# Kernel tuning notes

Measured on AMD Instinct MI355X. Metric: run time of the kernel, lower is better.

The kernel has to match this reference:

```python
import jax, jax.numpy as jnp
import numpy as np
import math

P = 7          # patch / kernel size (must be odd for onion-peeling: N = 1+4*m*(m+1) = P*P)
EPS = 1e-6
EPS_W = 0.5

def _ball_dirs():
    u = [np.array([[1.0, 0.0]])]
    s = [np.zeros(1)]
    for k in range(1, P // 2 + 1):
        n = 8 * k
        th = np.linspace(0.0, 2.0 * math.pi * (1.0 - 1.0 / n), n)
        u.append(np.stack([np.cos(th), np.sin(th)], 1))
        s.append(np.full(n, k / (P // 2)))
    return (np.concatenate(u, 0).astype(np.float32), np.concatenate(s).astype(np.float32))

_U, _S = _ball_dirs()  # [N,2], [N], N == P*P == 49

def _forward(x, metric_w, metric_b, proj_w, proj_b):
    B, C, H, W = x.shape
    Hp, Wp = H // P, W // P
    u = jnp.asarray(_U)
    s = jnp.asarray(_S)
    # metric net: strided conv -> 7 params per patch
    params = jax.lax.conv_general_dilated(
        x, metric_w, (P, P), 'VALID',
        dimension_numbers=('NCHW', 'OIHW', 'NCHW')) + metric_b[None, :, None, None]
    v_raw = jnp.moveaxis(params[:, :2], 1, -1)                      # [B,Hp,Wp,2]
    v = v_raw / jnp.maximum(jnp.linalg.norm(v_raw, axis=-1, keepdims=True), 1e-12)
    eig = 2.0 * jax.nn.sigmoid(jnp.moveaxis(params[:, 2:4], 1, -1))  # [B,Hp,Wp,2]
    scale = 0.5 + 1.5 * jax.nn.sigmoid(jnp.moveaxis(params[:, 4:5], 1, -1))
    eig = eig * scale
    vp = jnp.stack([-v[..., 1], v[..., 0]], -1)
    R = jnp.stack([v, vp], -1)                                      # [B,Hp,Wp,2,2] (columns v, v_perp)
    M = R @ (eig[..., None] * jnp.swapaxes(R, -1, -2))              # R diag(eig) R^T
    w = params[:, 5:7]                                              # [B,2,Hp,Wp]
    w = w * (1.0 - EPS_W) * jax.nn.sigmoid(jnp.linalg.norm(w, axis=1, keepdims=True))
    # Finsler-Randers norm F(u) = sqrt(u^T M u + eps) + w.u for all N unit dirs
    quad = jnp.einsum('nj,bhwij,ni->bnhw', u, M, u)                 # [B,N,Hp,Wp]
    drift = jnp.einsum('bihw,ni->bnhw', w, u)
    F_u = jnp.sqrt(quad + EPS) + drift
    y = (u[None, :, :, None, None] / (F_u[:, :, None] + EPS)
         * s[None, :, None, None, None])                            # [B,N,2,Hp,Wp]
    y = y.reshape(B, P, P, 2, Hp, Wp)[:, :, :, ::-1]                # flip last coord pair (x,y)->(y,x)
    gi = jnp.arange(P, dtype=x.dtype) - P // 2
    grid = jnp.stack(jnp.meshgrid(gi, gi, indexing='ij'), -1)       # [P,P,2]
    off = y - grid[None, :, :, :, None, None]                       # [B,P,P,2,Hp,Wp]
    off_y = jnp.transpose(off[:, :, :, 0], (0, 3, 4, 1, 2))         # [B,Hp,Wp,P,P]
    off_x = jnp.transpose(off[:, :, :, 1], (0, 3, 4, 1, 2))
    base_h = (jnp.arange(Hp, dtype=x.dtype) * P)[None, :, None, None, None]
    base_w = (jnp.arange(Wp, dtype=x.dtype) * P)[None, None, :, None, None]
    ki = jnp.arange(P, dtype=x.dtype)
    py = off_y + base_h + ki[None, None, None, :, None]             # sample rows
    px = off_x + base_w + ki[None, None, None, None, :]             # sample cols
    # bilinear sampling with zero padding (torchvision deform_conv2d semantics)
    y0 = jnp.floor(py)
    x0 = jnp.floor(px)
    wy = py - y0
    wx = px - x0

    def gather(yi, xi):
        valid = (yi >= 0) & (yi <= H - 1) & (xi >= 0) & (xi <= W - 1)
        yc = jnp.clip(yi, 0, H - 1).astype(jnp.int32)
        xc = jnp.clip(xi, 0, W - 1).astype(jnp.int32)
        vals = jax.vmap(lambda img, yy, xx: img[:, yy, xx])(x, yc, xc)  # [B,C,Hp,Wp,P,P]
        return vals * valid[:, None].astype(x.dtype)

    sampled = (gather(y0, x0) * ((1 - wy) * (1 - wx))[:, None]
               + gather(y0, x0 + 1) * ((1 - wy) * wx)[:, None]
               + gather(y0 + 1, x0) * (wy * (1 - wx))[:, None]
               + gather(y0 + 1, x0 + 1) * (wy * wx)[:, None])       # [B,C,Hp,Wp,P,P]
    out = jnp.einsum('bchwij,ecij->behw', sampled, proj_w) + proj_b[None, :, None, None]
    return jnp.moveaxis(out.reshape(B, out.shape[1], -1), 1, 2)     # [B, Hp*Wp, E]

def setup_inputs():
    key = jax.random.key(0)
    k0, k1, k2 = jax.random.split(key, 3)
    B, C, H, W, E = 64, 3, 224, 224, 384
    x = jax.random.normal(k0, (B, C, H, W), jnp.float32)
    metric_w = jax.random.normal(k1, (7, C, P, P), jnp.float32) / math.sqrt(C * P * P)
    metric_b = jnp.zeros((7,), jnp.float32)
    proj_w = jax.random.normal(k2, (E, C, P, P), jnp.float32) / (P * math.sqrt(C))
    proj_b = jnp.zeros((E,), jnp.float32)
    return {"x": x, "metric_w": metric_w, "metric_b": metric_b,
            "proj_w": proj_w, "proj_b": proj_b}

def reference(x, metric_w, metric_b, proj_w, proj_b):
    return _forward(x, metric_w, metric_b, proj_w, proj_b)
```

## Files before the change

### kernel.cpp

```cpp
#include <hip/hip_runtime.h>
#include <math.h>

#define PP   7
#define NDIR 49
#define CIN  3
#define KK   147
#define KPAD 160
#define EE   384
#define HH   224
#define WW   224
#define GG   16
#define TB   256
#define NPX  112
#define WSTR 208
#define SROW 164
#define SSTR 17

typedef __attribute__((ext_vector_type(8))) __bf16 bf16x8;
typedef __attribute__((ext_vector_type(4))) float  f32x4;

__device__ __forceinline__ float sigmoidf_(float v) {
    return 1.0f / (1.0f + expf(-v));
}

__global__ void pack_kernel(const float* __restrict__ x,
                            const float* __restrict__ pw,
                            const float* __restrict__ mw,
                            float* __restrict__ xp,
                            unsigned short* __restrict__ pwB,
                            float* __restrict__ mwg,
                            int npix4) {
    int idx = blockIdx.x * blockDim.x + threadIdx.x;
    if (idx < EE * KPAD) {
        int e = idx / KPAD;
        int k = idx - e * KPAD;
        float v = (k < KK) ? pw[e * KK + k] : 0.0f;
        __bf16 h = (__bf16)v;
        pwB[idx] = *(unsigned short*)&h;
    }
    if (idx < 7 * WSTR) {
        int prm = idx / WSTR, r = idx - prm * WSTR;
        float v = 0.0f;
        if (r < 196) {
            int q = r >> 2, c = r & 3;
            if (c < 3) v = mw[prm * KK + c * 49 + q];
        }
        mwg[idx] = v;
    }
    if (idx < npix4) {
        const int ppi = HH * WW / 4;
        int b = idx / ppi;
        int p = (idx - b * ppi) * 4;
        const float* xb = x + (size_t)b * (CIN * HH * WW) + p;
        f32x4 r0 = *(const f32x4*)(xb);
        f32x4 r1 = *(const f32x4*)(xb + HH * WW);
        f32x4 r2 = *(const f32x4*)(xb + 2 * HH * WW);
        float* op = xp + ((size_t)b * (HH * WW) + p) * 4;
        #pragma unroll
        for (int i = 0; i < 4; ++i) {
            f32x4 v = {r0[i], r1[i], r2[i], 0.0f};
            *(f32x4*)(op + i * 4) = v;
        }
    }
}

__launch_bounds__(TB, 8)
__global__ void fused_kernel(const float* __restrict__ xp,
                             const float* __restrict__ mwg,
                             const float* __restrict__ mb,
                             const unsigned short* __restrict__ pwB,
                             const float* __restrict__ pb,
                             float* __restrict__ out) {
    __shared__ __align__(16) float mwp_s[7 * WSTR];
    __shared__ float dirs[NDIR][3];
    __shared__ float par_s[GG][8];
    __shared__ float der_s[GG][5];
    __shared__ __align__(16) float buf[3136];

    const int t   = threadIdx.x;
    const int blk = blockIdx.x;
    const int b   = blk >> 6;
    const int rem = blk & 63;
    const int hp  = rem >> 1;
    const int wp0 = (rem & 1) * GG;
    const size_t m0 = (size_t)blk * GG;
    const int row0 = hp * PP;
    const int col0 = wp0 * PP;

    for (int i4 = t; i4 < 7 * WSTR / 4; i4 += TB)
        *(f32x4*)&mwp_s[i4 * 4] = *(const f32x4*)&mwg[i4 * 4];
    if (t >= 64 && t < 64 + NDIR) {
        int n = t - 64;
        float u0, u1, s;
        if (n == 0)      { u0 = 1.0f; u1 = 0.0f; s = 0.0f; }
        else if (n < 9)  { float th = (float)(n - 1)  * 0.78539816339744831f; u0 = cosf(th); u1 = sinf(th); s = 0.33333334f; }
        else if (n < 25) { float th = (float)(n - 9)  * 0.39269908169872414f; u0 = cosf(th); u1 = sinf(th); s = 0.66666669f; }
        else             { float th = (float)(n - 25) * 0.26179938779914941f; u0 = cosf(th); u1 = sinf(th); s = 1.0f; }
        dirs[n][0] = u0; dirs[n][1] = u1; dirs[n][2] = s;
    }

    const size_t pbase = (size_t)b * (HH * WW);
    for (int item = t; item < 7 * NPX; item += TB) {
        int i = item / NPX, px = item - i * NPX;
        f32x4 v = *(const f32x4*)(xp + (pbase + (size_t)(row0 + i) * WW + col0 + px) * 4);
        *(f32x4*)&buf[item * 4] = v;
    }
    __syncthreads();

    if (t < 112) {
        int prm = t >> 4, g = t & 15;
        const float* wrow = &mwp_s[prm * WSTR];
        float acc0 = 0.0f, acc1 = 0.0f, acc2 = 0.0f;
        #pragma unroll 1
        for (int i = 0; i < 7; ++i) {
            const float* bp = &buf[(i * NPX + g * 7) * 4];
            const float* wp = &wrow[i * 28];
            #pragma unroll
            for (int j = 0; j < 7; ++j) {
                f32x4 pix = *(const f32x4*)&bp[j * 4];
                f32x4 w4  = *(const f32x4*)&wp[j * 4];
                acc0 = fmaf(pix[0], w4[0], acc0);
                acc1 = fmaf(pix[1], w4[1], acc1);
                acc2 = fmaf(pix[2], w4[2], acc2);
            }
        }
        par_s[g][prm] = mb[prm] + acc0 + acc1 + acc2;
    }
    __syncthreads();

    if (t < GG) {
        float a0 = par_s[t][0], a1 = par_s[t][1], a2 = par_s[t][2], a3 = par_s[t][3];
        float a4 = par_s[t][4], a5 = par_s[t][5], a6 = par_s[t][6];
        float nrm = sqrtf(a0 * a0 + a1 * a1);
        float inv = 1.0f / fmaxf(nrm, 1e-12f);
        float v0 = a0 * inv, v1 = a1 * inv;
        float e0 = 2.0f * sigmoidf_(a2);
        float e1 = 2.0f * sigmoidf_(a3);
        float sc = 0.5f + 1.5f * sigmoidf_(a4);
        e0 *= sc; e1 *= sc;
        float wn  = sqrtf(a5 * a5 + a6 * a6);
        float wsc = 0.5f * sigmoidf_(wn);
        der_s[t][0] = e0 * v0 * v0 + e1 * v1 * v1;
        der_s[t][1] = (e0 - e1) * v0 * v1;
        der_s[t][2] = e0 * v1 * v1 + e1 * v0 * v0;
        der_s[t][3] = a5 * wsc;
        der_s[t][4] = a6 * wsc;
    }
    for (int z = t; z < GG * (SROW - KK); z += TB) {
        int g = z / (SROW - KK), r = z - g * (SROW - KK);
        buf[g * SROW + KK + r] = 0.0f;
    }
    __syncthreads();

    for (int item = t; item < GG * NDIR; item += TB) {
        int g = item / NDIR;
        int n = item - g * NDIR;
        float u0 = dirs[n][0], u1 = dirs[n][1], s = dirs[n][2];
        float M00 = der_s[g][0], M01 = der_s[g][1], M11 = der_s[g][2];
        float w0 = der_s[g][3], w1 = der_s[g][4];
        float quad  = u0 * u0 * M00 + 2.0f * u0 * u1 * M01 + u1 * u1 * M11;
        float drift = w0 * u0 + w1 * u1;
        float F = sqrtf(quad + 1e-6f) + drift;
        float r = s / (F + 1e-6f);
        float py = (float)(row0 + 3) + u1 * r;
        float px = (float)(col0 + g * PP + 3) + u0 * r;
        float y0f = floorf(py), x0f = floorf(px);
        float y1f = y0f + 1.0f, x1f = x0f + 1.0f;
        float wy = py - y0f, wx = px - x0f;
        float c00 = (1.0f - wy) * (1.0f - wx);
        float c01 = (1.0f - wy) * wx;
        float c10 = wy * (1.0f - wx);
        float c11 = wy * wx;
        bool vy0 = (y0f >= 0.0f) && (y0f <= (float)(HH - 1));
        bool vy1 = (y1f >= 0.0f) && (y1f <= (float)(HH - 1));
        bool vx0 = (x0f >= 0.0f) && (x0f <= (float)(WW - 1));
        bool vx1 = (x1f >= 0.0f) && (x1f <= (float)(WW - 1));
        c00 *= (vy0 && vx0) ? 1.0f : 0.0f;
        c01 *= (vy0 && vx1) ? 1.0f : 0.0f;
        c10 *= (vy1 && vx0) ? 1.0f : 0.0f;
        c11 *= (vy1 && vx1) ? 1.0f : 0.0f;
        int iy0 = (int)fminf(fmaxf(y0f, 0.0f), (float)(HH - 1));
        int iy1 = (int)fminf(fmaxf(y1f, 0.0f), (float)(HH - 1));
        int ix0 = (int)fminf(fmaxf(x0f, 0.0f), (float)(WW - 1));
        int ix1 = (int)fminf(fmaxf(x1f, 0.0f), (float)(WW - 1));
        f32x4 q00 = *(const f32x4*)(xp + (pbase + (size_t)(iy0 * WW + ix0)) * 4);
        f32x4 q01 = *(const f32x4*)(xp + (pbase + (size_t)(iy0 * WW + ix1)) * 4);
        f32x4 q10 = *(const f32x4*)(xp + (pbase + (size_t)(iy1 * WW + ix0)) * 4);
        f32x4 q11 = *(const f32x4*)(xp + (pbase + (size_t)(iy1 * WW + ix1)) * 4);
        #pragma unroll
        for (int c = 0; c < CIN; ++c) {
            buf[g * SROW + c * NDIR + n] =
                q00[c] * c00 + q01[c] * c01 + q10[c] * c10 + q11[c] * c11;
        }
    }
    __syncthreads();

    const int lane = t & 63;
    const int wv   = t >> 6;
    const int nrow = lane & 15;
    const int hi   = lane >> 4;

    bf16x8 sfr[5];
    const float* srow = &buf[nrow * SROW];
    #pragma unroll
    for (int ks = 0; ks < 5; ++ks) {
        f32x4 lo = *(const f32x4*)&srow[ks * 32 + hi * 8];
        f32x4 hv = *(const f32x4*)&srow[ks * 32 + hi * 8 + 4];
        #pragma unroll
        for (int j = 0; j < 4; ++j) sfr[ks][j] = (__bf16)lo[j];
        #pragma unroll
        for (int j = 0; j < 4; ++j) sfr[ks][4 + j] = (__bf16)hv[j];
    }

    float* orow = out + (m0 + nrow) * EE;
    #pragma unroll
    for (int q = 0; q < 6; ++q) {
        int tile = wv * 6 + q;
        int erow = tile * 16 + nrow;
        const unsigned short* arow = pwB + (size_t)erow * KPAD + hi * 8;
        f32x4 acc = {0.0f, 0.0f, 0.0f, 0.0f};
        #pragma unroll
        for (int ks = 0; ks < 5; ++ks) {
            bf16x8 afr = *(const bf16x8*)&arow[ks * 32];
            acc = __builtin_amdgcn_mfma_f32_16x16x32_bf16(afr, sfr[ks], acc, 0, 0, 0);
        }
        int e0 = tile * 16 + hi * 4;
        f32x4 b4 = *(const f32x4*)&pb[e0];
        f32x4 o = acc + b4;
        *(f32x4*)&orow[e0] = o;
    }
}

__launch_bounds__(TB, 6)
__global__ void fused_planar_kernel(const float* __restrict__ x,
                                    const float* __restrict__ mw,
                                    const float* __restrict__ mb,
                                    const unsigned short* __restrict__ pwB,
                                    const float* __restrict__ pb,
                                    float* __restrict__ out) {
    __shared__ float mws[7 * KK];
    __shared__ float dirs[NDIR][3];
    __shared__ float par_s[GG][8];
    __shared__ float der_s[GG][5];
    __shared__ __align__(16) float buf[2512];

    const int t   = threadIdx.x;
    const int blk = blockIdx.x;
    const int b   = blk >> 6;
    const int rem = blk & 63;
    const int hp  = rem >> 1;
    const int wp0 = (rem & 1) * GG;
    const size_t m0 = (size_t)blk * GG;
    const int row0 = hp * PP;
    const int col0 = wp0 * PP;
    const float* xb = x + (size_t)b * (CIN * HH * WW);

    for (int i = t; i < 7 * KK; i += TB) mws[i] = mw[i];
    if (t >= 64 && t < 64 + NDIR) {
        int n = t - 64;
        float u0, u1, s;
        if (n == 0)      { u0 = 1.0f; u1 = 0.0f; s = 0.0f; }
        else if (n < 9)  { float th = (float)(n - 1)  * 0.78539816339744831f; u0 = cosf(th); u1 = sinf(th); s = 0.33333334f; }
        else if (n < 25) { float th = (float)(n - 9)  * 0.39269908169872414f; u0 = cosf(th); u1 = sinf(th); s = 0.66666669f; }
        else             { float th = (float)(n - 25) * 0.26179938779914941f; u0 = cosf(th); u1 = sinf(th); s = 1.0f; }
        dirs[n][0] = u0; dirs[n][1] = u1; dirs[n][2] = s;
    }
    for (int item = t; item < CIN * 7 * NPX; item += TB) {
        int c = item / (7 * NPX), r2 = item - c * (7 * NPX);
        int i = r2 / NPX, px = r2 - i * NPX;
        buf[item] = xb[(size_t)c * (HH * WW) + (size_t)(row0 + i) * WW + col0 + px];
    }
    __syncthreads();
    if (t < 112) {
        int prm = t >> 4, g = t & 15;
        const float* wrow = &mws[prm * KK];
        float acc0 = 0.0f, acc1 = 0.0f, acc2 = 0.0f;
        #pragma unroll 1
        for (int i = 0; i < 7; ++i) {
            const float* b0 = &buf[(0 * 7 + i) * NPX + g * 7];
            const float* b1 = &buf[(1 * 7 + i) * NPX + g * 7];
            const float* b2 = &buf[(2 * 7 + i) * NPX + g * 7];
            #pragma unroll
            for (int j = 0; j < 7; ++j) {
                acc0 = fmaf(b0[j], wrow[i * 7 + j], acc0);
                acc1 = fmaf(b1[j], wrow[49 + i * 7 + j], acc1);
                acc2 = fmaf(b2[j], wrow[98 + i * 7 + j], acc2);
            }
        }
        par_s[g][prm] = mb[prm] + acc0 + acc1 + acc2;
    }
    __syncthreads();
    if (t < GG) {
        float a0 = par_s[t][0], a1 = par_s[t][1], a2 = par_s[t][2], a3 = par_s[t][3];
        float a4 = par_s[t][4], a5 = par_s[t][5], a6 = par_s[t][6];
        float nrm = sqrtf(a0 * a0 + a1 * a1);
        float inv = 1.0f / fmaxf(nrm, 1e-12f);
        float v0 = a0 * inv, v1 = a1 * inv;
        float e0 = 2.0f * sigmoidf_(a2);
        float e1 = 2.0f * sigmoidf_(a3);
        float sc = 0.5f + 1.5f * sigmoidf_(a4);
        e0 *= sc; e1 *= sc;
        float wn  = sqrtf(a5 * a5 + a6 * a6);
        float wsc = 0.5f * sigmoidf_(wn);
        der_s[t][0] = e0 * v0 * v0 + e1 * v1 * v1;
        der_s[t][1] = (e0 - e1) * v0 * v1;
        der_s[t][2] = e0 * v1 * v1 + e1 * v0 * v0;
        der_s[t][3] = a5 * wsc;
        der_s[t][4] = a6 * wsc;
    }
    __syncthreads();
    for (int item = t; item < GG * NDIR; item += TB) {
        int g = item / NDIR;
        int n = item - g * NDIR;
        float u0 = dirs[n][0], u1 = dirs[n][1], s = dirs[n][2];
        float M00 = der_s[g][0], M01 = der_s[g][1], M11 = der_s[g][2];
        float w0 = der_s[g][3], w1 = der_s[g][4];
        float quad  = u0 * u0 * M00 + 2.0f * u0 * u1 * M01 + u1 * u1 * M11;
        float drift = w0 * u0 + w1 * u1;
        float F = sqrtf(quad + 1e-6f) + drift;
        float r = s / (F + 1e-6f);
        float py = (float)(row0 + 3) + u1 * r;
        float px = (float)(col0 + g * PP + 3) + u0 * r;
        float y0f = floorf(py), x0f = floorf(px);
        float y1f = y0f + 1.0f, x1f = x0f + 1.0f;
        float wy = py - y0f, wx = px - x0f;
        float c00 = (1.0f - wy) * (1.0f - wx);
        float c01 = (1.0f - wy) * wx;
        float c10 = wy * (1.0f - wx);
        float c11 = wy * wx;
        bool vy0 = (y0f >= 0.0f) && (y0f <= (float)(HH - 1));
        bool vy1 = (y1f >= 0.0f) && (y1f <= (float)(HH - 1));
        bool vx0 = (x0f >= 0.0f) && (x0f <= (float)(WW - 1));
        bool vx1 = (x1f >= 0.0f) && (x1f <= (float)(WW - 1));
        c00 *= (vy0 && vx0) ? 1.0f : 0.0f;
        c01 *= (vy0 && vx1) ? 1.0f : 0.0f;
        c10 *= (vy1 && vx0) ? 1.0f : 0.0f;
        c11 *= (vy1 && vx1) ? 1.0f : 0.0f;
        int iy0 = (int)fminf(fmaxf(y0f, 0.0f), (float)(HH - 1));
        int iy1 = (int)fminf(fmaxf(y1f, 0.0f), (float)(HH - 1));
        int ix0 = (int)fminf(fmaxf(x0f, 0.0f), (float)(WW - 1));
        int ix1 = (int)fminf(fmaxf(x1f, 0.0f), (float)(WW - 1));
        int o00 = iy0 * WW + ix0, o01 = iy0 * WW + ix1;
        int o10 = iy1 * WW + ix0, o11 = iy1 * WW + ix1;
        #pragma unroll
        for (int c = 0; c < CIN; ++c) {
            const float* xc = xb + c * (HH * WW);
            buf[(c * NDIR + n) * SSTR + g] =
                xc[o00] * c00 + xc[o01] * c01 + xc[o10] * c10 + xc[o11] * c11;
        }
    }
    __syncthreads();
    const int lane = t & 63;
    const int wv   = t >> 6;
    const int nrow = lane & 15;
    const int hi   = lane >> 4;
    bf16x8 sfr[5];
    #pragma unroll
    for (int ks = 0; ks < 5; ++ks) {
        #pragma unroll
        for (int j = 0; j < 8; ++j) {
            int k = ks * 32 + hi * 8 + j;
            float v = (k < KK) ? buf[k * SSTR + nrow] : 0.0f;
            sfr[ks][j] = (__bf16)v;
        }
    }
    float* orow = out + (m0 + nrow) * EE;
    #pragma unroll
    for (int q = 0; q < 6; ++q) {
        int tile = wv * 6 + q;
        int erow = tile * 16 + nrow;
        const unsigned short* arow = pwB + (size_t)erow * KPAD + hi * 8;
        f32x4 acc = {0.0f, 0.0f, 0.0f, 0.0f};
        #pragma unroll
        for (int ks = 0; ks < 5; ++ks) {
            bf16x8 afr = *(const bf16x8*)&arow[ks * 32];
            acc = __builtin_amdgcn_mfma_f32_16x16x32_bf16(afr, sfr[ks], acc, 0, 0, 0);
        }
        int e0 = tile * 16 + hi * 4;
        f32x4 b4 = *(const f32x4*)&pb[e0];
        f32x4 o = acc + b4;
        *(f32x4*)&orow[e0] = o;
    }
}

extern "C" void kernel_launch(void* const* d_in, const int* in_sizes, int n_in,
                              void* d_out, int out_size, void* d_ws, size_t ws_size,
                              hipStream_t stream) {
    const float* x  = (const float*)d_in[0];
    const float* mw = (const float*)d_in[1];
    const float* mb = (const float*)d_in[2];
    const float* pw = (const float*)d_in[3];
    const float* pb = (const float*)d_in[4];
    float* out = (float*)d_out;

    unsigned short* pwB = (unsigned short*)d_ws;
    float* mwg = (float*)((char*)d_ws + (size_t)(EE * KPAD) * 2);
    float* xp  = (float*)((char*)d_ws + (size_t)(1 << 17));

    const int B = in_sizes[0] / (CIN * HH * WW);
    const int npix = B * HH * WW;
    const int npix4 = npix / 4;
    const size_t need = (size_t)(1 << 17) + (size_t)npix * 4 * sizeof(float);
    const bool packed = ws_size >= need;

    if (packed) {
        int grid = (npix4 > EE * KPAD ? npix4 : EE * KPAD);
        pack_kernel<<<(grid + 255) / 256, 256, 0, stream>>>(x, pw, mw, xp, pwB, mwg, npix4);
        fused_kernel<<<B * 64, TB, 0, stream>>>(xp, mwg, mb, pwB, pb, out);
    } else {
        pack_kernel<<<(EE * KPAD + 255) / 256, 256, 0, stream>>>(x, pw, mw, xp, pwB, mwg, 0);
        fused_planar_kernel<<<B * 64, TB, 0, stream>>>(x, mw, mb, pwB, pb, out);
    }
}
```

Measured before the change: 204.2 us.

## Make each wavefront own four patches to drop block-wide barriers

Each wavefront now loads its own 7x28 pixel strip into its private region of shared memory. It also computes the metric conv for its four patches and their derived parameters, then does the bilinear sampling, so three of the four __syncthreads are removed. Metric weights are read directly from global memory instead of being staged in shared memory, and the direction table is computed inline with fast __cosf/__sinf instead of a shared lookup. The approach relies on implicit wavefront-lockstep ordering between par_s/der_s/buf writes and reads without explicit barriers or fences. It also uses slightly less accurate trig.

Result: slower. 214.9 us (+5.2%).

```diff
diff --git a/kernel.cpp b/kernel.cpp
--- a/kernel.cpp
+++ b/kernel.cpp
@@ -14,6 +14,7 @@
 #define NPX  112
 #define WSTR 208
 #define SROW 164
+#define WREG 784
 #define SSTR 17
 
 typedef __attribute__((ext_vector_type(8))) __bf16 bf16x8;
@@ -71,66 +72,65 @@
                              const unsigned short* __restrict__ pwB,
                              const float* __restrict__ pb,
                              float* __restrict__ out) {
-    __shared__ __align__(16) float mwp_s[7 * WSTR];
-    __shared__ float dirs[NDIR][3];
     __shared__ float par_s[GG][8];
     __shared__ float der_s[GG][5];
-    __shared__ __align__(16) float buf[3136];
-
-    const int t   = threadIdx.x;
-    const int blk = blockIdx.x;
-    const int b   = blk >> 6;
-    const int rem = blk & 63;
-    const int hp  = rem >> 1;
-    const int wp0 = (rem & 1) * GG;
+    __shared__ __align__(16) float buf[4 * WREG];
+
+    const int t    = threadIdx.x;
+    const int lane = t & 63;
+    const int wv   = t >> 6;
+    const int blk  = blockIdx.x;
+    const int b    = blk >> 6;
+    const int rem  = blk & 63;
+    const int hp   = rem >> 1;
+    const int wp0  = (rem & 1) * GG;
     const size_t m0 = (size_t)blk * GG;
     const int row0 = hp * PP;
     const int col0 = wp0 * PP;
-
-    for (int i4 = t; i4 < 7 * WSTR / 4; i4 += TB)
-        *(f32x4*)&mwp_s[i4 * 4] = *(const f32x4*)&mwg[i4 * 4];
-    if (t >= 64 && t < 64 + NDIR) {
-        int n = t - 64;
-        float u0, u1, s;
-        if (n == 0)      { u0 = 1.0f; u1 = 0.0f; s = 0.0f; }
-        else if (n < 9)  { float th = (float)(n - 1)  * 0.78539816339744831f; u0 = cosf(th); u1 = sinf(th); s = 0.33333334f; }
-        else if (n < 25) { float th = (float)(n - 9)  * 0.39269908169872414f; u0 = cosf(th); u1 = sinf(th); s = 0.66666669f; }
-        else             { float th = (float)(n - 25) * 0.26179938779914941f; u0 = cosf(th); u1 = sinf(th); s = 1.0f; }
-        dirs[n][0] = u0; dirs[n][1] = u1; dirs[n][2] = s;
-    }
+    const int wbase = wv * WREG;
 
     const size_t pbase = (size_t)b * (HH * WW);
-    for (int item = t; item < 7 * NPX; item += TB) {
-        int i = item / NPX, px = item - i * NPX;
-        f32x4 v = *(const f32x4*)(xp + (pbase + (size_t)(row0 + i) * WW + col0 + px) * 4);
-        *(f32x4*)&buf[item * 4] = v;
-    }
-    __syncthreads();
-
-    if (t < 112) {
-        int prm = t >> 4, g = t & 15;
-        const float* wrow = &mwp_s[prm * WSTR];
-        float acc0 = 0.0f, acc1 = 0.0f, acc2 = 0.0f;
-        #pragma unroll 1
-        for (int i = 0; i < 7; ++i) {
-            const float* bp = &buf[(i * NPX + g * 7) * 4];
-            const float* wp = &wrow[i * 28];
-            #pragma unroll
-            for (int j = 0; j < 7; ++j) {
-                f32x4 pix = *(const f32x4*)&bp[j * 4];
-                f32x4 w4  = *(const f32x4*)&wp[j * 4];
-                acc0 = fmaf(pix[0], w4[0], acc0);
-                acc1 = fmaf(pix[1], w4[1], acc1);
-                acc2 = fmaf(pix[2], w4[2], acc2);
+
+    const int colw = col0 + wv * 28;
+    #pragma unroll
+    for (int r = 0; r < 4; ++r) {
+        int idx = r * 64 + lane;
+        if (idx < 196) {
+            int i = idx / 28, j28 = idx - i * 28;
+            f32x4 v = *(const f32x4*)(xp + (pbase + (size_t)(row0 + i) * WW + colw + j28) * 4);
+            *(f32x4*)&buf[wbase + idx * 4] = v;
+        }
+    }
+
+    if (lane < 56) {
+        int d = lane >> 1, h = lane & 1;
+        int prm = d >> 2, gl = d & 3;
+        const float* wq = mwg + prm * WSTR;
+        const float* pq = &buf[wbase + gl * 28];
+        float a0 = 0.0f, a1 = 0.0f, a2 = 0.0f;
+        #pragma unroll 5
+        for (int it = 0; it < 25; ++it) {
+            int q = it * 2 + h;
+            if (q < 49) {
+                int i = q / 7, j = q - i * 7;
+                f32x4 pix = *(const f32x4*)&pq[i * 112 + j * 4];
+                f32x4 w4  = *(const f32x4*)&wq[q * 4];
+                a0 = fmaf(pix[0], w4[0], a0);
+                a1 = fmaf(pix[1], w4[1], a1);
+                a2 = fmaf(pix[2], w4[2], a2);
             }
         }
-        par_s[g][prm] = mb[prm] + acc0 + acc1 + acc2;
-    }
-    __syncthreads();
-
-    if (t < GG) {
-        float a0 = par_s[t][0], a1 = par_s[t][1], a2 = par_s[t][2], a3 = par_s[t][3];
-        float a4 = par_s[t][4], a5 = par_s[t][5], a6 = par_s[t][6];
+        float a = a0 + a1 + a2;
+        a += __shfl_xor(a, 1);
+        par_s[wv * 4 + gl][prm] = a;
+    }
+
+    if (lane < 4) {
+        int g = wv * 4 + lane;
+        float a0 = par_s[g][0] + mb[0], a1 = par_s[g][1] + mb[1];
+        float a2 = par_s[g][2] + mb[2], a3 = par_s[g][3] + mb[3];
+        float a4 = par_s[g][4] + mb[4], a5 = par_s[g][5] + mb[5];
+        float a6 = par_s[g][6] + mb[6];
         float nrm = sqrtf(a0 * a0 + a1 * a1);
         float inv = 1.0f / fmaxf(nrm, 1e-12f);
         float v0 = a0 * inv, v1 = a1 * inv;
@@ -140,68 +140,77 @@
         e0 *= sc; e1 *= sc;
         float wn  = sqrtf(a5 * a5 + a6 * a6);
         float wsc = 0.5f * sigmoidf_(wn);
-        der_s[t][0] = e0 * v0 * v0 + e1 * v1 * v1;
-        der_s[t][1] = (e0 - e1) * v0 * v1;
-        der_s[t][2] = e0 * v1 * v1 + e1 * v0 * v0;
-        der_s[t][3] = a5 * wsc;
-        der_s[t][4] = a6 * wsc;
-    }
-    for (int z = t; z < GG * (SROW - KK); z += TB) {
-        int g = z / (SROW - KK), r = z - g * (SROW - KK);
-        buf[g * SROW + KK + r] = 0.0f;
-    }
+        der_s[g][0] = e0 * v0 * v0 + e1 * v1 * v1;
+        der_s[g][1] = (e0 - e1) * v0 * v1;
+        der_s[g][2] = e0 * v1 * v1 + e1 * v0 * v0;
+        der_s[g][3] = a5 * wsc;
+        der_s[g][4] = a6 * wsc;
+    }
+
+    for (int z = lane; z < 4 * (SROW - KK); z += 64) {
+        int rw = z / (SROW - KK), kk = z - rw * (SROW - KK);
+        buf[wbase + rw * SROW + KK + kk] = 0.0f;
+    }
+
+    #pragma unroll
+    for (int r = 0; r < 4; ++r) {
+        int idx = r * 64 + lane;
+        if (idx < 196) {
+            int gl = idx / 49, n = idx - gl * 49;
+            int g  = wv * 4 + gl;
+            float bs, st, sv;
+            if (n >= 25)     { bs = 25.0f; st = 0.26179938779914941f; sv = 1.0f; }
+            else if (n >= 9) { bs = 9.0f;  st = 0.39269908169872414f; sv = 0.66666669f; }
+            else if (n >= 1) { bs = 1.0f;  st = 0.78539816339744831f; sv = 0.33333334f; }
+            else             { bs = 0.0f;  st = 0.0f;                 sv = 0.0f; }
+            float th = ((float)n - bs) * st;
+            float u0 = __cosf(th), u1 = __sinf(th);
+            float M00 = der_s[g][0], M01 = der_s[g][1], M11 = der_s[g][2];
+            float w0 = der_s[g][3], w1 = der_s[g][4];
+            float quad  = u0 * u0 * M00 + 2.0f * u0 * u1 * M01 + u1 * u1 * M11;
+            float drift = w0 * u0 + w1 * u1;
+            float F = sqrtf(quad + 1e-6f) + drift;
+            float rr = sv / (F + 1e-6f);
+            float py = (float)(row0 + 3) + u1 * rr;
+            float px = (float)(col0 + g * PP + 3) + u0 * rr;
+            float y0f = floorf(py), x0f = floorf(px);
+            float y1f = y0f + 1.0f, x1f = x0f + 1.0f;
+            float wy = py - y0f, wx = px - x0f;
+            float c00 = (1.0f - wy) * (1.0f - wx);
+            float c01 = (1.0f - wy) * wx;
+            float c10 = wy * (1.0f - wx);
+            float c11 = wy * wx;
+            bool vy0 = (y0f >= 0.0f) && (y0f <= (float)(HH - 1));
+            bool vy1 = (y1f >= 0.0f) && (y1f <= (float)(HH - 1));
+            bool vx0 = (x0f >= 0.0f) && (x0f <= (float)(WW - 1));
+            bool vx1 = (x1f >= 0.0f) && (x1f <= (float)(WW - 1));
+            c00 *= (vy0 && vx0) ? 1.0f : 0.0f;
+            c01 *= (vy0 && vx1) ? 1.0f : 0.0f;
+            c10 *= (vy1 && vx0) ? 1.0f : 0.0f;
+            c11 *= (vy1 && vx1) ? 1.0f : 0.0f;
+            int iy0 = (int)fminf(fmaxf(y0f, 0.0f), (float)(HH - 1));
+            int iy1 = (int)fminf(fmaxf(y1f, 0.0f), (float)(HH - 1));
+            int ix0 = (int)fminf(fmaxf(x0f, 0.0f), (float)(WW - 1));
+            int ix1 = (int)fminf(fmaxf(x1f, 0.0f), (float)(WW - 1));
+            f32x4 q00 = *(const f32x4*)(xp + (pbase + (size_t)(iy0 * WW + ix0)) * 4);
+            f32x4 q01 = *(const f32x4*)(xp + (pbase + (size_t)(iy0 * WW + ix1)) * 4);
+            f32x4 q10 = *(const f32x4*)(xp + (pbase + (size_t)(iy1 * WW + ix0)) * 4);
+            f32x4 q11 = *(const f32x4*)(xp + (pbase + (size_t)(iy1 * WW + ix1)) * 4);
+            #pragma unroll
+            for (int c = 0; c < CIN; ++c) {
+                buf[wbase + gl * SROW + c * NDIR + n] =
+                    q00[c] * c00 + q01[c] * c01 + q10[c] * c10 + q11[c] * c11;
+            }
+        }
+    }
+
     __syncthreads();
 
-    for (int item = t; item < GG * NDIR; item += TB) {
-        int g = item / NDIR;
-        int n = item - g * NDIR;
-        float u0 = dirs[n][0], u1 = dirs[n][1], s = dirs[n][2];
-        float M00 = der_s[g][0], M01 = der_s[g][1], M11 = der_s[g][2];
-        float w0 = der_s[g][3], w1 = der_s[g][4];
-        float quad  = u0 * u0 * M00 + 2.0f * u0 * u1 * M01 + u1 * u1 * M11;
-        float drift = w0 * u0 + w1 * u1;
-        float F = sqrtf(quad + 1e-6f) + drift;
-        float r = s / (F + 1e-6f);
-        float py = (float)(row0 + 3) + u1 * r;
-        float px = (float)(col0 + g * PP + 3) + u0 * r;
-        float y0f = floorf(py), x0f = floorf(px);
-        float y1f = y0f + 1.0f, x1f = x0f + 1.0f;
-        float wy = py - y0f, wx = px - x0f;
-        float c00 = (1.0f - wy) * (1.0f - wx);
-        float c01 = (1.0f - wy) * wx;
-        float c10 = wy * (1.0f - wx);
-        float c11 = wy * wx;
-        bool vy0 = (y0f >= 0.0f) && (y0f <= (float)(HH - 1));
-        bool vy1 = (y1f >= 0.0f) && (y1f <= (float)(HH - 1));
-        bool vx0 = (x0f >= 0.0f) && (x0f <= (float)(WW - 1));
-        bool vx1 = (x1f >= 0.0f) && (x1f <= (float)(WW - 1));
-        c00 *= (vy0 && vx0) ? 1.0f : 0.0f;
-        c01 *= (vy0 && vx1) ? 1.0f : 0.0f;
-        c10 *= (vy1 && vx0) ? 1.0f : 0.0f;
-        c11 *= (vy1 && vx1) ? 1.0f : 0.0f;
-        int iy0 = (int)fminf(fmaxf(y0f, 0.0f), (float)(HH - 1));
-        int iy1 = (int)fminf(fmaxf(y1f, 0.0f), (float)(HH - 1));
-        int ix0 = (int)fminf(fmaxf(x0f, 0.0f), (float)(WW - 1));
-        int ix1 = (int)fminf(fmaxf(x1f, 0.0f), (float)(WW - 1));
-        f32x4 q00 = *(const f32x4*)(xp + (pbase + (size_t)(iy0 * WW + ix0)) * 4);
-        f32x4 q01 = *(const f32x4*)(xp + (pbase + (size_t)(iy0 * WW + ix1)) * 4);
-        f32x4 q10 = *(const f32x4*)(xp + (pbase + (size_t)(iy1 * WW + ix0)) * 4);
-        f32x4 q11 = *(const f32x4*)(xp + (pbase + (size_t)(iy1 * WW + ix1)) * 4);
-        #pragma unroll
-        for (int c = 0; c < CIN; ++c) {
-            buf[g * SROW + c * NDIR + n] =
-                q00[c] * c00 + q01[c] * c01 + q10[c] * c10 + q11[c] * c11;
-        }
-    }
-    __syncthreads();
-
-    const int lane = t & 63;
-    const int wv   = t >> 6;
     const int nrow = lane & 15;
     const int hi   = lane >> 4;
 
     bf16x8 sfr[5];
-    const float* srow = &buf[nrow * SROW];
+    const float* srow = &buf[(nrow >> 2) * WREG + (nrow & 3) * SROW];
     #pragma unroll
     for (int ks = 0; ks < 5; ++ks) {
         f32x4 lo = *(const f32x4*)&srow[ks * 32 + hi * 8];
```

## Move metric-net conv into pack kernel and stash derived params in packed pad lane

Applied to the files above, without the earlier changes.

The pixel-packing kernel now runs per strip: it loads the planar input into shared memory, computes the strided metric conv and the derived Finsler parameters there, and writes the interleaved pixels with those parameters stored in the otherwise unused fourth channel. The main kernel then reads the parameters back from that lane instead of re-reading the strip and redoing the conv, so it needs less shared memory. The sampled-patch buffer is also transposed to a k-major layout with stride 17, which changes bank access for both writes and the fragment loads. The trade-off is a heavier pack kernel with more syncs and scalar shared-memory reads when building the bf16 fragments.

New measurement: 196.5 us. 1.04x faster.

```diff
diff --git a/kernel.cpp b/kernel.cpp
--- a/kernel.cpp
+++ b/kernel.cpp
@@ -11,10 +11,8 @@
 #define WW   224
 #define GG   16
 #define TB   256
+#define SSTR 17
 #define NPX  112
-#define WSTR 208
-#define SROW 164
-#define SSTR 17
 
 typedef __attribute__((ext_vector_type(8))) __bf16 bf16x8;
 typedef __attribute__((ext_vector_type(4))) float  f32x4;
@@ -23,105 +21,60 @@
     return 1.0f / (1.0f + expf(-v));
 }
 
-__global__ void pack_kernel(const float* __restrict__ x,
-                            const float* __restrict__ pw,
-                            const float* __restrict__ mw,
-                            float* __restrict__ xp,
-                            unsigned short* __restrict__ pwB,
-                            float* __restrict__ mwg,
-                            int npix4) {
-    int idx = blockIdx.x * blockDim.x + threadIdx.x;
-    if (idx < EE * KPAD) {
-        int e = idx / KPAD;
-        int k = idx - e * KPAD;
+__launch_bounds__(TB, 6)
+__global__ void pack_strip_kernel(const float* __restrict__ x,
+                                  const float* __restrict__ pw,
+                                  const float* __restrict__ mw,
+                                  const float* __restrict__ mb,
+                                  float* __restrict__ xp,
+                                  unsigned short* __restrict__ pwB) {
+    __shared__ float mws[7 * KK];
+    __shared__ float par_s[GG][8];
+    __shared__ float der_s[GG][5];
+    __shared__ __align__(16) float buf[CIN * 7 * NPX];
+
+    const int t   = threadIdx.x;
+    const int blk = blockIdx.x;
+
+    int gidx = blk * TB + t;
+    if (gidx < EE * KPAD) {
+        int e = gidx / KPAD, k = gidx - e * KPAD;
         float v = (k < KK) ? pw[e * KK + k] : 0.0f;
         __bf16 h = (__bf16)v;
-        pwB[idx] = *(unsigned short*)&h;
-    }
-    if (idx < 7 * WSTR) {
-        int prm = idx / WSTR, r = idx - prm * WSTR;
-        float v = 0.0f;
-        if (r < 196) {
-            int q = r >> 2, c = r & 3;
-            if (c < 3) v = mw[prm * KK + c * 49 + q];
-        }
-        mwg[idx] = v;
-    }
-    if (idx < npix4) {
-        const int ppi = HH * WW / 4;
-        int b = idx / ppi;
-        int p = (idx - b * ppi) * 4;
-        const float* xb = x + (size_t)b * (CIN * HH * WW) + p;
-        f32x4 r0 = *(const f32x4*)(xb);
-        f32x4 r1 = *(const f32x4*)(xb + HH * WW);
-        f32x4 r2 = *(const f32x4*)(xb + 2 * HH * WW);
-        float* op = xp + ((size_t)b * (HH * WW) + p) * 4;
-        #pragma unroll
-        for (int i = 0; i < 4; ++i) {
-            f32x4 v = {r0[i], r1[i], r2[i], 0.0f};
-            *(f32x4*)(op + i * 4) = v;
-        }
-    }
-}
-
-__launch_bounds__(TB, 8)
-__global__ void fused_kernel(const float* __restrict__ xp,
-                             const float* __restrict__ mwg,
-                             const float* __restrict__ mb,
-                             const unsigned short* __restrict__ pwB,
-                             const float* __restrict__ pb,
-                             float* __restrict__ out) {
-    __shared__ __align__(16) float mwp_s[7 * WSTR];
-    __shared__ float dirs[NDIR][3];
-    __shared__ float par_s[GG][8];
-    __shared__ float der_s[GG][5];
-    __shared__ __align__(16) float buf[3136];
-
-    const int t   = threadIdx.x;
-    const int blk = blockIdx.x;
+        pwB[gidx] = *(unsigned short*)&h;
+    }
+
     const int b   = blk >> 6;
     const int rem = blk & 63;
     const int hp  = rem >> 1;
     const int wp0 = (rem & 1) * GG;
-    const size_t m0 = (size_t)blk * GG;
     const int row0 = hp * PP;
     const int col0 = wp0 * PP;
-
-    for (int i4 = t; i4 < 7 * WSTR / 4; i4 += TB)
-        *(f32x4*)&mwp_s[i4 * 4] = *(const f32x4*)&mwg[i4 * 4];
-    if (t >= 64 && t < 64 + NDIR) {
-        int n = t - 64;
-        float u0, u1, s;
-        if (n == 0)      { u0 = 1.0f; u1 = 0.0f; s = 0.0f; }
-        else if (n < 9)  { float th = (float)(n - 1)  * 0.78539816339744831f; u0 = cosf(th); u1 = sinf(th); s = 0.33333334f; }
-        else if (n < 25) { float th = (float)(n - 9)  * 0.39269908169872414f; u0 = cosf(th); u1 = sinf(th); s = 0.66666669f; }
-        else             { float th = (float)(n - 25) * 0.26179938779914941f; u0 = cosf(th); u1 = sinf(th); s = 1.0f; }
-        dirs[n][0] = u0; dirs[n][1] = u1; dirs[n][2] = s;
-    }
-
-    const size_t pbase = (size_t)b * (HH * WW);
-    for (int item = t; item < 7 * NPX; item += TB) {
-        int i = item / NPX, px = item - i * NPX;
-        f32x4 v = *(const f32x4*)(xp + (pbase + (size_t)(row0 + i) * WW + col0 + px) * 4);
-        *(f32x4*)&buf[item * 4] = v;
+    const float* xb = x + (size_t)b * (CIN * HH * WW);
+
+    for (int i = t; i < 7 * KK; i += TB) mws[i] = mw[i];
+    for (int qi = t; qi < 588; qi += TB) {
+        int c = qi / 196, r = qi - c * 196, i = r / 28, j = r - i * 28;
+        f32x4 v = *(const f32x4*)(xb + (size_t)c * (HH * WW)
+                                  + (size_t)(row0 + i) * WW + col0 + j * 4);
+        *(f32x4*)&buf[(c * 7 + i) * NPX + j * 4] = v;
     }
     __syncthreads();
 
     if (t < 112) {
         int prm = t >> 4, g = t & 15;
-        const float* wrow = &mwp_s[prm * WSTR];
+        const float* wrow = &mws[prm * KK];
         float acc0 = 0.0f, acc1 = 0.0f, acc2 = 0.0f;
         #pragma unroll 1
         for (int i = 0; i < 7; ++i) {
-            const float* bp = &buf[(i * NPX + g * 7) * 4];
-            const float* wp = &wrow[i * 28];
+            const float* b0 = &buf[(0 * 7 + i) * NPX + g * 7];
+            const float* b1 = &buf[(1 * 7 + i) * NPX + g * 7];
+            const float* b2 = &buf[(2 * 7 + i) * NPX + g * 7];
             #pragma unroll
             for (int j = 0; j < 7; ++j) {
-                f32x4 pix = *(const f32x4*)&bp[j * 4];
-                f32x4 w4  = *(const f32x4*)&wp[j * 4];
-                acc0 = fmaf(pix[0], w4[0], acc0);
-                acc1 = fmaf(pix[1], w4[1], acc1);
-                acc2 = fmaf(pix[2], w4[2], acc2);
+                acc0 = fmaf(b0[j], wrow[i * 7 + j], acc0);
+                acc1 = fmaf(b1[j], wrow[49 + i * 7 + j], acc1);
+                acc2 = fmaf(b2[j], wrow[98 + i * 7 + j], acc2);
             }
         }
         par_s[g][prm] = mb[prm] + acc0 + acc1 + acc2;
@@ -146,9 +99,52 @@
         der_s[t][3] = a5 * wsc;
         der_s[t][4] = a6 * wsc;
     }
-    for (int z = t; z < GG * (SROW - KK); z += TB) {
-        int g = z / (SROW - KK), r = z - g * (SROW - KK);
-        buf[g * SROW + KK + r] = 0.0f;
+    __syncthreads();
+
+    const size_t pbase = (size_t)b * (HH * WW);
+    for (int q = t; q < 7 * NPX; q += TB) {
+        int i = q / NPX, px = q - i * NPX;
+        float w = 0.0f;
+        if (i == 0 && px < 80) { int g5 = px / 5; w = der_s[g5][px - g5 * 5]; }
+        f32x4 v = { buf[(0 * 7 + i) * NPX + px],
+                    buf[(1 * 7 + i) * NPX + px],
+                    buf[(2 * 7 + i) * NPX + px], w };
+        *(f32x4*)(xp + (pbase + (size_t)(row0 + i) * WW + col0 + px) * 4) = v;
+    }
+}
+
+__launch_bounds__(TB, 8)
+__global__ void fused_kernel(const float* __restrict__ xp,
+                             const unsigned short* __restrict__ pwB,
+                             const float* __restrict__ pb,
+                             float* __restrict__ out) {
+    __shared__ float dirs[NDIR][3];
+    __shared__ float der_s[GG][5];
+    __shared__ __align__(16) float buf[KK * SSTR];
+
+    const int t   = threadIdx.x;
+    const int blk = blockIdx.x;
+    const int b   = blk >> 6;
+    const int rem = blk & 63;
+    const int hp  = rem >> 1;
+    const int wp0 = (rem & 1) * GG;
+    const size_t m0 = (size_t)blk * GG;
+    const int row0 = hp * PP;
+    const int col0 = wp0 * PP;
+    const size_t pbase = (size_t)b * (HH * WW);
+
+    if (t >= 64 && t < 64 + NDIR) {
+        int n = t - 64;
+        float u0, u1, s;
+        if (n == 0)      { u0 = 1.0f; u1 = 0.0f; s = 0.0f; }
+        else if (n < 9)  { float th = (float)(n - 1)  * 0.78539816339744831f; u0 = cosf(th); u1 = sinf(th); s = 0.33333334f; }
+        else if (n < 25) { float th = (float)(n - 9)  * 0.39269908169872414f; u0 = cosf(th); u1 = sinf(th); s = 0.66666669f; }
+        else             { float th = (float)(n - 25) * 0.26179938779914941f; u0 = cosf(th); u1 = sinf(th); s = 1.0f; }
+        dirs[n][0] = u0; dirs[n][1] = u1; dirs[n][2] = s;
+    }
+    if (t < 80) {
+        int g5 = t / 5;
+        der_s[g5][t - g5 * 5] = xp[(pbase + (size_t)row0 * WW + col0 + t) * 4 + 3];
     }
     __syncthreads();
 
@@ -189,7 +185,7 @@
         f32x4 q11 = *(const f32x4*)(xp + (pbase + (size_t)(iy1 * WW + ix1)) * 4);
         #pragma unroll
         for (int c = 0; c < CIN; ++c) {
-            buf[g * SROW + c * NDIR + n] =
+            buf[(c * NDIR + n) * SSTR + g] =
                 q00[c] * c00 + q01[c] * c01 + q10[c] * c10 + q11[c] * c11;
         }
     }
@@ -201,15 +197,14 @@
     const int hi   = lane >> 4;
 
     bf16x8 sfr[5];
-    const float* srow = &buf[nrow * SROW];
     #pragma unroll
     for (int ks = 0; ks < 5; ++ks) {
-        f32x4 lo = *(const f32x4*)&srow[ks * 32 + hi * 8];
-        f32x4 hv = *(const f32x4*)&srow[ks * 32 + hi * 8 + 4];
-        #pragma unroll
-        for (int j = 0; j < 4; ++j) sfr[ks][j] = (__bf16)lo[j];
-        #pragma unroll
-        for (int j = 0; j < 4; ++j) sfr[ks][4 + j] = (__bf16)hv[j];
+        #pragma unroll
+        for (int j = 0; j < 8; ++j) {
+            int k = ks * 32 + hi * 8 + j;
+            float v = (k < KK) ? buf[k * SSTR + nrow] : 0.0f;
+            sfr[ks][j] = (__bf16)v;
+        }
     }
 
     float* orow = out + (m0 + nrow) * EE;
@@ -228,6 +223,17 @@
         f32x4 b4 = *(const f32x4*)&pb[e0];
         f32x4 o = acc + b4;
         *(f32x4*)&orow[e0] = o;
+    }
+}
+
+__global__ void pack_pw_kernel(const float* __restrict__ pw, unsigned short* __restrict__ pwB) {
+    int idx = blockIdx.x * blockDim.x + threadIdx.x;
+    if (idx < EE * KPAD) {
+        int e = idx / KPAD;
+        int k = idx - e * KPAD;
+        float v = (k < KK) ? pw[e * KK + k] : 0.0f;
+        __bf16 h = (__bf16)v;
+        pwB[idx] = *(unsigned short*)&h;
     }
 }
 
@@ -394,21 +400,18 @@
     float* out = (float*)d_out;
 
     unsigned short* pwB = (unsigned short*)d_ws;
-    float* mwg = (float*)((char*)d_ws + (size_t)(EE * KPAD) * 2);
-    float* xp  = (float*)((char*)d_ws + (size_t)(1 << 17));
+    float* xp = (float*)((char*)d_ws + (size_t)(1 << 17));
 
     const int B = in_sizes[0] / (CIN * HH * WW);
     const int npix = B * HH * WW;
-    const int npix4 = npix / 4;
     const size_t need = (size_t)(1 << 17) + (size_t)npix * 4 * sizeof(float);
     const bool packed = ws_size >= need;
 
     if (packed) {
-        int grid = (npix4 > EE * KPAD ? npix4 : EE * KPAD);
-        pack_kernel<<<(grid + 255) / 256, 256, 0, stream>>>(x, pw, mw, xp, pwB, mwg, npix4);
-        fused_kernel<<<B * 64, TB, 0, stream>>>(xp, mwg, mb, pwB, pb, out);
+        pack_strip_kernel<<<B * 64, TB, 0, stream>>>(x, pw, mw, mb, xp, pwB);
+        fused_kernel<<<B * 64, TB, 0, stream>>>(xp, pwB, pb, out);
     } else {
-        pack_kernel<<<(EE * KPAD + 255) / 256, 256, 0, stream>>>(x, pw, mw, xp, pwB, mwg, 0);
+        pack_pw_kernel<<<(EE * KPAD + 255) / 256, 256, 0, stream>>>(pw, pwB);
         fused_planar_kernel<<<B * 64, TB, 0, stream>>>(x, mw, mb, pwB, pb, out);
     }
 }
```
